# Performance work log

Hardware: AMD Instinct MI355X
Metric: run time of the kernel (lower is better)

Reference implementation:

```python
import jax, jax.numpy as jnp
import numpy as np

N_NODES = 50000
N_EDGES = 800000
IN_CH = 128
HID = 64
HEADS = 4
OUT_CH = 10
NUM_GRAPHS = 500
NEG_SLOPE = 0.2  # PyG GATConv default LeakyReLU slope


def gat_conv(x, src, dst, W, a_src, a_dst, b, concat):
    """One PyG-style GATConv (inference; attention dropout disabled).
    x: [N, F_in], src/dst: [E'] (self-loops already appended).
    W: [F_in, H*C], a_src/a_dst: [H, C], b: [H*C] or [C].
    """
    N = x.shape[0]
    H, C = a_src.shape
    h = (x @ W).reshape(N, H, C)                      # [N,H,C]
    al_s = jnp.einsum('nhc,hc->nh', h, a_src)          # [N,H]
    al_d = jnp.einsum('nhc,hc->nh', h, a_dst)          # [N,H]
    e = al_s[src] + al_d[dst]                          # [E,H]
    e = jnp.where(e > 0, e, NEG_SLOPE * e)             # leaky_relu
    # segment softmax over edges sharing the same destination node
    e_max = jax.ops.segment_max(e, dst, num_segments=N)
    ex = jnp.exp(e - e_max[dst])
    denom = jax.ops.segment_sum(ex, dst, num_segments=N)
    alpha = ex / (denom[dst] + 1e-16)                  # [E,H]
    msg = h[src] * alpha[:, :, None]                   # [E,H,C]
    out = jax.ops.segment_sum(msg, dst, num_segments=N)  # [N,H,C]
    out = out.reshape(N, H * C) if concat else out.mean(axis=1)
    return out + b


def _forward(x, edge_index, batch, W1, a_src1, a_dst1, b1,
             W2, a_src2, a_dst2, b2, fc_w, fc_b):
    N = x.shape[0]
    loops = jnp.arange(N, dtype=edge_index.dtype)
    src = jnp.concatenate([edge_index[0], loops])
    dst = jnp.concatenate([edge_index[1], loops])
    h = gat_conv(x, src, dst, W1, a_src1, a_dst1, b1, concat=True)
    h = jax.nn.relu(h)                                  # dropout: eval mode
    h = gat_conv(h, src, dst, W2, a_src2, a_dst2, b2, concat=False)
    pooled = jax.ops.segment_sum(h, batch, num_segments=NUM_GRAPHS)  # global_add_pool
    logits = pooled @ fc_w + fc_b
    return jax.nn.log_softmax(logits, axis=1)


def setup_inputs() -> dict:
    key = jax.random.key(0)
    ks = jax.random.split(key, 12)
    g = lambda k, shp, fan: jax.random.normal(k, shp, dtype=jnp.float32) * (1.0 / np.sqrt(fan))
    x = jax.random.normal(ks[0], (N_NODES, IN_CH), dtype=jnp.float32)
    edge_index = jax.random.randint(ks[1], (2, N_EDGES), 0, N_NODES, dtype=jnp.int64)
    batch = jnp.sort(jax.random.randint(ks[2], (N_NODES,), 0, NUM_GRAPHS, dtype=jnp.int64))
    return {
        'x': x,
        'edge_index': edge_index,
        'batch': batch,
        'W1': g(ks[3], (IN_CH, HEADS * HID), IN_CH),
        'a_src1': g(ks[4], (HEADS, HID), HID),
        'a_dst1': g(ks[5], (HEADS, HID), HID),
        'b1': jnp.zeros((HEADS * HID,), dtype=jnp.float32),
        'W2': g(ks[6], (HEADS * HID, HID), HEADS * HID),
        'a_src2': g(ks[7], (1, HID), HID),
        'a_dst2': g(ks[8], (1, HID), HID),
        'b2': jnp.zeros((HID,), dtype=jnp.float32),
        'fc_w': g(ks[9], (HID, OUT_CH), HID),
        'fc_b': jnp.zeros((OUT_CH,), dtype=jnp.float32),
    }


def reference(x, edge_index, batch, W1, a_src1, a_dst1, b1,
              W2, a_src2, a_dst2, b2, fc_w, fc_b):
    return _forward(x, edge_index, batch, W1, a_src1, a_dst1, b1,
                    W2, a_src2, a_dst2, b2, fc_w, fc_b)
```

## Files before the change

kernel.cpp:

```cpp
#include <hip/hip_runtime.h>
#include <hip/hip_fp16.h>
#include <math.h>

#define N_NODES   50000
#define N_EDGES   800000
#define IN_CH     128
#define HID       64
#define HEADS     4
#define F1        (HEADS * HID)
#define OUT_CH    10
#define NUM_GRAPHS 500
#define NEG_SLOPE 0.2f
#define RPAD      132
#define NTILES    (N_NODES / 16)
#define CAP       64

typedef __attribute__((ext_vector_type(8))) _Float16 half8;
typedef __attribute__((ext_vector_type(4))) float floatx4;

__device__ __forceinline__ unsigned short f2h(float f) {
    _Float16 h = (_Float16)f;
    unsigned short u; __builtin_memcpy(&u, &h, 2); return u;
}
__device__ __forceinline__ unsigned int pack_h2(float lo, float hi) {
    auto r = __builtin_amdgcn_cvt_pkrtz(lo, hi);
    unsigned int u; __builtin_memcpy(&u, &r, 4); return u;
}
__device__ __forceinline__ float h2f(unsigned short u) {
    _Float16 h; __builtin_memcpy(&h, &u, 2); return (float)h;
}

__global__ void init_kernel(int* __restrict__ cnt, unsigned short* __restrict__ csr,
                            const float* __restrict__ W1, unsigned short* __restrict__ W1p,
                            const float* __restrict__ W2, unsigned short* __restrict__ W2p)
{
    const int gid = blockIdx.x * blockDim.x + threadIdx.x;
    if (gid < N_NODES) {
        cnt[gid] = 1;
        csr[gid * CAP] = (unsigned short)gid;
    }
    if (gid < 4096) {
        const int t = gid >> 8, kt = (gid >> 6) & 3, l = gid & 63;
        const int col = t * 16 + (l & 15);
        unsigned short* o = W1p + (size_t)((t * 4 + kt) * 64 + l) * 8;
        #pragma unroll
        for (int j = 0; j < 8; ++j) {
            const int k = kt * 32 + (l >> 4) * 8 + j;
            o[j] = f2h(W1[k * F1 + col]);
        }
    } else if (gid < 6144) {
        const int g2 = gid - 4096;
        const int t = g2 >> 9, kt = (g2 >> 6) & 7, l = g2 & 63;
        const int col = t * 16 + (l & 15);
        unsigned short* o = W2p + (size_t)((t * 8 + kt) * 64 + l) * 8;
        #pragma unroll
        for (int j = 0; j < 8; ++j) {
            const int k = kt * 32 + (l >> 4) * 8 + j;
            o[j] = f2h(W2[k * HID + col]);
        }
    }
}

__global__ __launch_bounds__(256) void scatter_gemm1(
    const int* __restrict__ ei, int* __restrict__ cnt,
    unsigned short* __restrict__ csr,
    const float* __restrict__ x, const unsigned short* __restrict__ W1p,
    const float* __restrict__ a_src1, const float* __restrict__ a_dst1,
    unsigned short* __restrict__ H1b,
    float* __restrict__ al_s1, float* __restrict__ al_d1)
{
    const int e = blockIdx.x * 256 + threadIdx.x;
    const int src = ei[e];
    const int dst = ei[N_EDGES + e];
    const int slot = atomicAdd(&cnt[dst], 1);

    const int m0 = blockIdx.x * 16;
    const int w = threadIdx.x >> 6;
    const int l = threadIdx.x & 63;
    const int q = l >> 4, r = l & 15;
    floatx4 acc[4] = {};
    const float* arow = x + (size_t)(m0 + r) * IN_CH + q * 8;
    #pragma unroll
    for (int kt = 0; kt < 4; ++kt) {
        const float4 f0 = *(const float4*)(arow + kt * 32);
        const float4 f1 = *(const float4*)(arow + kt * 32 + 4);
        union { uint4 u; half8 h; } a;
        a.u = make_uint4(pack_h2(f0.x, f0.y), pack_h2(f0.z, f0.w),
                         pack_h2(f1.x, f1.y), pack_h2(f1.z, f1.w));
        #pragma unroll
        for (int t = 0; t < 4; ++t) {
            const int nt = w * 4 + t;
            const half8 b = *(const half8*)(W1p + (size_t)((nt * 4 + kt) * 64 + l) * 8);
            acc[t] = __builtin_amdgcn_mfma_f32_16x16x32_f16(a.h, b, acc[t], 0, 0, 0);
        }
    }
    float ls[4] = {0.f, 0.f, 0.f, 0.f}, ld[4] = {0.f, 0.f, 0.f, 0.f};
    #pragma unroll
    for (int t = 0; t < 4; ++t) {
        const int col = (w * 4 + t) * 16 + r;
        const float as = a_src1[col], ad = a_dst1[col];
        #pragma unroll
        for (int reg = 0; reg < 4; ++reg) {
            H1b[(size_t)(m0 + q * 4 + reg) * F1 + col] = f2h(acc[t][reg]);
            ls[reg] += acc[t][reg] * as;
            ld[reg] += acc[t][reg] * ad;
        }
    }
    #pragma unroll
    for (int reg = 0; reg < 4; ++reg) {
        #pragma unroll
        for (int off = 8; off > 0; off >>= 1) {
            ls[reg] += __shfl_down(ls[reg], off, 16);
            ld[reg] += __shfl_down(ld[reg], off, 16);
        }
    }
    if (r == 0) {
        #pragma unroll
        for (int reg = 0; reg < 4; ++reg) {
            const int n = m0 + q * 4 + reg;
            al_s1[n * HEADS + w] = ls[reg];
            al_d1[n * HEADS + w] = ld[reg];
        }
    }

    if (slot < CAP) csr[dst * CAP + slot] = (unsigned short)src;
}

__global__ __launch_bounds__(256) void agg1_gemm2(
    const int* __restrict__ cnt, const unsigned short* __restrict__ csr,
    const float* __restrict__ al_s1, const float* __restrict__ al_d1,
    const uint2* __restrict__ H1b2, const float* __restrict__ b1,
    const unsigned short* __restrict__ W2p,
    const float* __restrict__ a_src2, const float* __restrict__ a_dst2,
    unsigned short* __restrict__ H2b,
    float* __restrict__ al_s2, float* __restrict__ al_d2)
{
    const int m0 = blockIdx.x * 16;
    const int w = threadIdx.x >> 6;
    const int l = threadIdx.x & 63;
    const char* H1base = (const char*)H1b2;
    __shared__ unsigned int rows[16][RPAD];
    __shared__ unsigned int sofs[16][CAP];
    __shared__ uint2        wtp[16][CAP];

    int nreg[4];
    #pragma unroll
    for (int d = 0; d < 4; ++d) {
        const int dd = w * 4 + d;
        const int dstn = m0 + dd;
        const int n = min(cnt[dstn], CAP);
        nreg[d] = n;
        const float4 ad = *(const float4*)(al_d1 + dstn * 4);
        float w0 = 0.f, w1 = 0.f, w2 = 0.f, w3 = 0.f;
        unsigned int off = 0;
        if (l < n) {
            const int s = csr[dstn * CAP + l];
            off = (unsigned int)s << 9;
            const float4 as = *(const float4*)(al_s1 + s * 4);
            float t0 = as.x + ad.x; t0 = t0 > 0.f ? t0 : NEG_SLOPE * t0;
            float t1 = as.y + ad.y; t1 = t1 > 0.f ? t1 : NEG_SLOPE * t1;
            float t2 = as.z + ad.z; t2 = t2 > 0.f ? t2 : NEG_SLOPE * t2;
            float t3 = as.w + ad.w; t3 = t3 > 0.f ? t3 : NEG_SLOPE * t3;
            w0 = __expf(t0); w1 = __expf(t1); w2 = __expf(t2); w3 = __expf(t3);
        }
        sofs[dd][l] = off;
        wtp[dd][l] = make_uint2(pack_h2(w0, w1), pack_h2(w2, w3));
    }
    __syncthreads();

    const int hf = l >> 5;
    const int ll = l & 31;
    const int hh = ll >> 3;
    const unsigned int lane16 = (unsigned int)(ll * 16);
    const float4 bb0 = *(const float4*)(b1 + 8 * ll);
    const float4 bb4 = *(const float4*)(b1 + 8 * ll + 4);
    #pragma unroll 1
    for (int d = 0; d < 4; ++d) {
        const int dd = w * 4 + d;
        const int n = nreg[d];
        float a0=0.f,a1=0.f,a2=0.f,a3=0.f,a4=0.f,a5=0.f,a6=0.f,a7=0.f,den=0.f;
        const int n8 = (n + 7) & ~7;
        for (int i = 0; i < n8; i += 8) {
            unsigned int off[4]; float wt[4];
            #pragma unroll
            for (int j = 0; j < 4; ++j) {
                const int slot = i + 2 * j + hf;
                off[j] = sofs[dd][slot];
                const uint2 wp = wtp[dd][slot];
                const unsigned int uw = (hh & 2) ? wp.y : wp.x;
                wt[j] = h2f((hh & 1) ? (unsigned short)(uw >> 16)
                                     : (unsigned short)(uw & 0xFFFFu));
            }
            uint4 u[4];
            #pragma unroll
            for (int j = 0; j < 4; ++j)
                u[j] = *(const uint4*)(H1base + (off[j] + lane16));
            #pragma unroll
            for (int j = 0; j < 4; ++j) {
                union { uint4 v; _Float16 hv[8]; } c; c.v = u[j];
                a0 += wt[j] * (float)c.hv[0];
                a1 += wt[j] * (float)c.hv[1];
                a2 += wt[j] * (float)c.hv[2];
                a3 += wt[j] * (float)c.hv[3];
                a4 += wt[j] * (float)c.hv[4];
                a5 += wt[j] * (float)c.hv[5];
                a6 += wt[j] * (float)c.hv[6];
                a7 += wt[j] * (float)c.hv[7];
                den += wt[j];
            }
        }
        a0 += __shfl_xor(a0, 32, 64);
        a1 += __shfl_xor(a1, 32, 64);
        a2 += __shfl_xor(a2, 32, 64);
        a3 += __shfl_xor(a3, 32, 64);
        a4 += __shfl_xor(a4, 32, 64);
        a5 += __shfl_xor(a5, 32, 64);
        a6 += __shfl_xor(a6, 32, 64);
        a7 += __shfl_xor(a7, 32, 64);
        den += __shfl_xor(den, 32, 64);
        if (l < 32) {
            const float rcp = 1.f / (den + 1e-16f);
            float v0 = fmaxf(a0 * rcp + bb0.x, 0.f);
            float v1 = fmaxf(a1 * rcp + bb0.y, 0.f);
            float v2 = fmaxf(a2 * rcp + bb0.z, 0.f);
            float v3 = fmaxf(a3 * rcp + bb0.w, 0.f);
            float v4 = fmaxf(a4 * rcp + bb4.x, 0.f);
            float v5 = fmaxf(a5 * rcp + bb4.y, 0.f);
            float v6 = fmaxf(a6 * rcp + bb4.z, 0.f);
            float v7 = fmaxf(a7 * rcp + bb4.w, 0.f);
            *(uint4*)&rows[dd][4 * ll] = make_uint4(pack_h2(v0, v1), pack_h2(v2, v3),
                                                    pack_h2(v4, v5), pack_h2(v6, v7));
        }
    }
    __syncthreads();

    const int q = l >> 4, r = l & 15;
    floatx4 acc = {};
    #pragma unroll
    for (int kt = 0; kt < 8; ++kt) {
        union { uint4 u; half8 hh2; } a;
        a.u = *(const uint4*)&rows[r][kt * 16 + q * 4];
        const half8 b = *(const half8*)(W2p + (size_t)((w * 8 + kt) * 64 + l) * 8);
        acc = __builtin_amdgcn_mfma_f32_16x16x32_f16(a.hh2, b, acc, 0, 0, 0);
    }
    const int col = w * 16 + r;
    const float as = a_src2[col], ad2 = a_dst2[col];
    float ls[4], ld[4];
    #pragma unroll
    for (int reg = 0; reg < 4; ++reg) {
        H2b[(size_t)(m0 + q * 4 + reg) * HID + col] = f2h(acc[reg]);
        ls[reg] = acc[reg] * as;
        ld[reg] = acc[reg] * ad2;
    }
    #pragma unroll
    for (int reg = 0; reg < 4; ++reg) {
        #pragma unroll
        for (int off = 8; off > 0; off >>= 1) {
            ls[reg] += __shfl_down(ls[reg], off, 16);
            ld[reg] += __shfl_down(ld[reg], off, 16);
        }
    }
    __shared__ float Ls[4][16], Ld[4][16];
    if (r == 0) {
        #pragma unroll
        for (int reg = 0; reg < 4; ++reg) {
            Ls[w][q * 4 + reg] = ls[reg];
            Ld[w][q * 4 + reg] = ld[reg];
        }
    }
    __syncthreads();
    if (threadIdx.x < 16) {
        const int row = threadIdx.x;
        al_s2[m0 + row] = Ls[0][row] + Ls[1][row] + Ls[2][row] + Ls[3][row];
        al_d2[m0 + row] = Ld[0][row] + Ld[1][row] + Ld[2][row] + Ld[3][row];
    }
}

__global__ __launch_bounds__(256) void agg2_csr(
    const int* __restrict__ cnt, const unsigned short* __restrict__ csr,
    const float* __restrict__ al_s2, const float* __restrict__ al_d2,
    const uint2* __restrict__ H2b2, uint2* __restrict__ out2b)
{
    const int dst = blockIdx.x * 4 + (threadIdx.x >> 6);
    const int l = threadIdx.x & 63;
    const int qt = l >> 4, j = l & 15;
    const int n = min(cnt[dst], CAP);
    const float ad = al_d2[dst];
    float a0 = 0.f, a1 = 0.f, a2 = 0.f, a3 = 0.f, den = 0.f;
    int s_reg = 0;
    float w_reg = 0.f;
    if (l < n) {
        s_reg = csr[dst * CAP + l];
        float t = al_s2[s_reg] + ad;
        t = t > 0.f ? t : NEG_SLOPE * t;
        w_reg = __expf(t);
    }
    const int n8 = (n + 7) & ~7;
    for (int i = 0; i < n8; i += 8) {
        const int e0 = i + qt, e1 = i + 4 + qt;
        const int   src0 = __shfl(s_reg, e0, 64), src1 = __shfl(s_reg, e1, 64);
        const float wt0  = __shfl(w_reg, e0, 64), wt1  = __shfl(w_reg, e1, 64);
        const uint2 u0 = H2b2[(size_t)src0 * (HID / 4) + j];
        const uint2 u1 = H2b2[(size_t)src1 * (HID / 4) + j];
        union { uint2 v; _Float16 hv[4]; } c0, c1; c0.v = u0; c1.v = u1;
        a0 += wt0 * (float)c0.hv[0] + wt1 * (float)c1.hv[0];
        a1 += wt0 * (float)c0.hv[1] + wt1 * (float)c1.hv[1];
        a2 += wt0 * (float)c0.hv[2] + wt1 * (float)c1.hv[2];
        a3 += wt0 * (float)c0.hv[3] + wt1 * (float)c1.hv[3];
        den += wt0 + wt1;
    }
    #pragma unroll
    for (int m = 16; m <= 32; m <<= 1) {
        a0 += __shfl_xor(a0, m, 64);
        a1 += __shfl_xor(a1, m, 64);
        a2 += __shfl_xor(a2, m, 64);
        a3 += __shfl_xor(a3, m, 64);
        den += __shfl_xor(den, m, 64);
    }
    if (l < 16) {
        const float rcp = 1.f / (den + 1e-16f);
        out2b[(size_t)dst * (HID / 4) + j] =
            make_uint2(pack_h2(a0 * rcp, a1 * rcp), pack_h2(a2 * rcp, a3 * rcp));
    }
}

__global__ __launch_bounds__(256) void pool_fc_kernel(
    const unsigned short* __restrict__ out2b, const float* __restrict__ b2,
    const int* __restrict__ batch,
    const float* __restrict__ fc_w, const float* __restrict__ fc_b,
    float* __restrict__ out)
{
    const int g = blockIdx.x;
    const int q = threadIdx.x >> 6, c = threadIdx.x & 63;
    __shared__ int se[2];
    __shared__ float partial[4][HID];
    __shared__ float pl[HID];
    __shared__ float logits[OUT_CH];
    if (threadIdx.x < 2) {
        const int target = g + threadIdx.x;
        int lo = 0, hi = N_NODES;
        while (lo < hi) { int mid = (lo + hi) >> 1; if (batch[mid] < target) lo = mid + 1; else hi = mid; }
        se[threadIdx.x] = lo;
    }
    __syncthreads();
    const int start = se[0], end = se[1];
    float acc = 0.f;
    for (int n = start + q; n < end; n += 4)
        acc += h2f(out2b[(size_t)n * HID + c]);
    partial[q][c] = acc;
    __syncthreads();
    if (q == 0)
        pl[c] = partial[0][c] + partial[1][c] + partial[2][c] + partial[3][c]
              + (float)(end - start) * b2[c];
    __syncthreads();
    if (threadIdx.x < OUT_CH) {
        float lg = fc_b[threadIdx.x];
        #pragma unroll
        for (int k = 0; k < HID; ++k) lg += pl[k] * fc_w[k * OUT_CH + threadIdx.x];
        logits[threadIdx.x] = lg;
    }
    __syncthreads();
    if (threadIdx.x == 0) {
        float m = logits[0];
        #pragma unroll
        for (int j2 = 1; j2 < OUT_CH; ++j2) m = fmaxf(m, logits[j2]);
        float s = 0.f;
        #pragma unroll
        for (int j2 = 0; j2 < OUT_CH; ++j2) s += __expf(logits[j2] - m);
        const float lse = m + __logf(s);
        #pragma unroll
        for (int j2 = 0; j2 < OUT_CH; ++j2) out[g * OUT_CH + j2] = logits[j2] - lse;
    }
}


extern "C" void kernel_launch(void* const* d_in, const int* in_sizes, int n_in,
                              void* d_out, int out_size, void* d_ws, size_t ws_size,
                              hipStream_t stream)
{
    const float* x      = (const float*)d_in[0];
    const int*   ei     = (const int*)  d_in[1];
    const int*   batch  = (const int*)  d_in[2];
    const float* W1     = (const float*)d_in[3];
    const float* a_src1 = (const float*)d_in[4];
    const float* a_dst1 = (const float*)d_in[5];
    const float* b1     = (const float*)d_in[6];
    const float* W2     = (const float*)d_in[7];
    const float* a_src2 = (const float*)d_in[8];
    const float* a_dst2 = (const float*)d_in[9];
    const float* b2     = (const float*)d_in[10];
    const float* fc_w   = (const float*)d_in[11];
    const float* fc_b   = (const float*)d_in[12];
    float* out = (float*)d_out;

    char* ws = (char*)d_ws;
    size_t off = 0;
    auto alloc_b = [&](size_t bytes) { void* p = (void*)(ws + off); off += (bytes + 15) & ~15ull; return p; };

    unsigned short* H1b  = (unsigned short*)alloc_b((size_t)N_NODES * F1 * 2);
    float* al_s1  = (float*)alloc_b((size_t)N_NODES * HEADS * 4);
    float* al_d1  = (float*)alloc_b((size_t)N_NODES * HEADS * 4);
    unsigned short* H2b  = (unsigned short*)alloc_b((size_t)N_NODES * HID * 2);
    float* al_s2  = (float*)alloc_b((size_t)N_NODES * 4);
    float* al_d2  = (float*)alloc_b((size_t)N_NODES * 4);
    unsigned short* out2b = (unsigned short*)alloc_b((size_t)N_NODES * HID * 2);
    int*   cnt    = (int*)alloc_b((size_t)N_NODES * 4);
    unsigned short* csr = (unsigned short*)alloc_b((size_t)N_NODES * CAP * 2);
    unsigned short* W1p = (unsigned short*)alloc_b((size_t)IN_CH * F1 * 2);
    unsigned short* W2p = (unsigned short*)alloc_b((size_t)F1 * HID * 2);

    init_kernel<<<(N_NODES + 255) / 256, 256, 0, stream>>>(cnt, csr, W1, W1p, W2, W2p);

    scatter_gemm1<<<NTILES, 256, 0, stream>>>(ei, cnt, csr, x, W1p,
                                              a_src1, a_dst1, H1b, al_s1, al_d1);

    agg1_gemm2<<<N_NODES / 16, 256, 0, stream>>>(cnt, csr, al_s1, al_d1,
                                                 (const uint2*)H1b, b1,
                                                 W2p, a_src2, a_dst2,
                                                 H2b, al_s2, al_d2);

    agg2_csr<<<N_NODES / 4, 256, 0, stream>>>(cnt, csr, al_s2, al_d2,
                                              (const uint2*)H2b, (uint2*)out2b);

    pool_fc_kernel<<<NUM_GRAPHS, 256, 0, stream>>>(out2b, b2, batch, fc_w, fc_b, out);
}
```

Baseline: 233.5 us.

## Split per-destination edge buckets into eight segments to spread atomic contention

The single per-node counter and 64-slot adjacency bucket become eight segments, each holding 16 slots, selected by the scatter block index, so atomics on the same destination spread across separate counters. Both aggregation kernels now read eight counters, build a prefix sum, and map each lane to its segment and slot. This aims to cut atomic serialization in the scatter phase. The cost is eight counter loads per destination, a larger initialization, and the risk of dropping edges when one segment exceeds 16 entries.

```diff
diff --git a/kernel.cpp b/kernel.cpp
--- a/kernel.cpp
+++ b/kernel.cpp
@@ -13,7 +13,8 @@
 #define NEG_SLOPE 0.2f
 #define RPAD      132
 #define NTILES    (N_NODES / 16)
-#define CAP       64
+#define NSEG      8
+#define SCAP      16
 
 typedef __attribute__((ext_vector_type(8))) _Float16 half8;
 typedef __attribute__((ext_vector_type(4))) float floatx4;
@@ -30,14 +31,17 @@
     _Float16 h; __builtin_memcpy(&h, &u, 2); return (float)h;
 }
 
-__global__ void init_kernel(int* __restrict__ cnt, unsigned short* __restrict__ csr,
+__global__ void init_kernel(int* __restrict__ cnt2, unsigned short* __restrict__ csr2,
                             const float* __restrict__ W1, unsigned short* __restrict__ W1p,
                             const float* __restrict__ W2, unsigned short* __restrict__ W2p)
 {
     const int gid = blockIdx.x * blockDim.x + threadIdx.x;
     if (gid < N_NODES) {
-        cnt[gid] = 1;
-        csr[gid * CAP] = (unsigned short)gid;
+        const int sseg = gid & 7;
+        #pragma unroll
+        for (int xx = 0; xx < NSEG; ++xx)
+            cnt2[xx * N_NODES + gid] = (xx == sseg) ? 1 : 0;
+        csr2[(sseg * N_NODES + gid) << 4] = (unsigned short)gid;
     }
     if (gid < 4096) {
         const int t = gid >> 8, kt = (gid >> 6) & 3, l = gid & 63;
@@ -62,17 +66,18 @@
 }
 
 __global__ __launch_bounds__(256) void scatter_gemm1(
-    const int* __restrict__ ei, int* __restrict__ cnt,
-    unsigned short* __restrict__ csr,
+    const int* __restrict__ ei, int* __restrict__ cnt2,
+    unsigned short* __restrict__ csr2,
     const float* __restrict__ x, const unsigned short* __restrict__ W1p,
     const float* __restrict__ a_src1, const float* __restrict__ a_dst1,
     unsigned short* __restrict__ H1b,
     float* __restrict__ al_s1, float* __restrict__ al_d1)
 {
     const int e = blockIdx.x * 256 + threadIdx.x;
+    const int seg = blockIdx.x & 7;
     const int src = ei[e];
     const int dst = ei[N_EDGES + e];
-    const int slot = atomicAdd(&cnt[dst], 1);
+    const int slot = atomicAdd(&cnt2[seg * N_NODES + dst], 1);
 
     const int m0 = blockIdx.x * 16;
     const int w = threadIdx.x >> 6;
@@ -123,11 +128,11 @@
         }
     }
 
-    if (slot < CAP) csr[dst * CAP + slot] = (unsigned short)src;
+    if (slot < SCAP) csr2[((seg * N_NODES + dst) << 4) + slot] = (unsigned short)src;
 }
 
 __global__ __launch_bounds__(256) void agg1_gemm2(
-    const int* __restrict__ cnt, const unsigned short* __restrict__ csr,
+    const int* __restrict__ cnt2, const unsigned short* __restrict__ csr2,
     const float* __restrict__ al_s1, const float* __restrict__ al_d1,
     const uint2* __restrict__ H1b2, const float* __restrict__ b1,
     const unsigned short* __restrict__ W2p,
@@ -140,21 +145,29 @@
     const int l = threadIdx.x & 63;
     const char* H1base = (const char*)H1b2;
     __shared__ unsigned int rows[16][RPAD];
-    __shared__ unsigned int sofs[16][CAP];
-    __shared__ uint2        wtp[16][CAP];
+    __shared__ unsigned int sofs[16][64];
+    __shared__ uint2        wtp[16][64];
 
     int nreg[4];
     #pragma unroll
     for (int d = 0; d < 4; ++d) {
         const int dd = w * 4 + d;
         const int dstn = m0 + dd;
-        const int n = min(cnt[dstn], CAP);
+        int pre[NSEG + 1]; pre[0] = 0;
+        #pragma unroll
+        for (int xx = 0; xx < NSEG; ++xx)
+            pre[xx + 1] = pre[xx] + min(cnt2[xx * N_NODES + dstn], SCAP);
+        const int n = min(pre[NSEG], 64);
         nreg[d] = n;
         const float4 ad = *(const float4*)(al_d1 + dstn * 4);
         float w0 = 0.f, w1 = 0.f, w2 = 0.f, w3 = 0.f;
         unsigned int off = 0;
         if (l < n) {
-            const int s = csr[dstn * CAP + l];
+            int x = 0, pb = 0;
+            #pragma unroll
+            for (int yy = 1; yy < NSEG; ++yy)
+                if (l >= pre[yy]) { x = yy; pb = pre[yy]; }
+            const int s = csr2[((x * N_NODES + dstn) << 4) + (l - pb)];
             off = (unsigned int)s << 9;
             const float4 as = *(const float4*)(al_s1 + s * 4);
             float t0 = as.x + ad.x; t0 = t0 > 0.f ? t0 : NEG_SLOPE * t0;
@@ -277,20 +290,28 @@
 }
 
 __global__ __launch_bounds__(256) void agg2_csr(
-    const int* __restrict__ cnt, const unsigned short* __restrict__ csr,
+    const int* __restrict__ cnt2, const unsigned short* __restrict__ csr2,
     const float* __restrict__ al_s2, const float* __restrict__ al_d2,
     const uint2* __restrict__ H2b2, uint2* __restrict__ out2b)
 {
     const int dst = blockIdx.x * 4 + (threadIdx.x >> 6);
     const int l = threadIdx.x & 63;
     const int qt = l >> 4, j = l & 15;
-    const int n = min(cnt[dst], CAP);
+    int pre[NSEG + 1]; pre[0] = 0;
+    #pragma unroll
+    for (int xx = 0; xx < NSEG; ++xx)
+        pre[xx + 1] = pre[xx] + min(cnt2[xx * N_NODES + dst], SCAP);
+    const int n = min(pre[NSEG], 64);
     const float ad = al_d2[dst];
     float a0 = 0.f, a1 = 0.f, a2 = 0.f, a3 = 0.f, den = 0.f;
     int s_reg = 0;
     float w_reg = 0.f;
     if (l < n) {
-        s_reg = csr[dst * CAP + l];
+        int x = 0, pb = 0;
+        #pragma unroll
+        for (int yy = 1; yy < NSEG; ++yy)
+            if (l >= pre[yy]) { x = yy; pb = pre[yy]; }
+        s_reg = csr2[((x * N_NODES + dst) << 4) + (l - pb)];
         float t = al_s2[s_reg] + ad;
         t = t > 0.f ? t : NEG_SLOPE * t;
         w_reg = __expf(t);
@@ -404,22 +425,22 @@
     float* al_s2  = (float*)alloc_b((size_t)N_NODES * 4);
     float* al_d2  = (float*)alloc_b((size_t)N_NODES * 4);
     unsigned short* out2b = (unsigned short*)alloc_b((size_t)N_NODES * HID * 2);
-    int*   cnt    = (int*)alloc_b((size_t)N_NODES * 4);
-    unsigned short* csr = (unsigned short*)alloc_b((size_t)N_NODES * CAP * 2);
+    int*   cnt2   = (int*)alloc_b((size_t)NSEG * N_NODES * 4);
+    unsigned short* csr2 = (unsigned short*)alloc_b((size_t)NSEG * N_NODES * SCAP * 2);
     unsigned short* W1p = (unsigned short*)alloc_b((size_t)IN_CH * F1 * 2);
     unsigned short* W2p = (unsigned short*)alloc_b((size_t)F1 * HID * 2);
 
-    init_kernel<<<(N_NODES + 255) / 256, 256, 0, stream>>>(cnt, csr, W1, W1p, W2, W2p);
-
-    scatter_gemm1<<<NTILES, 256, 0, stream>>>(ei, cnt, csr, x, W1p,
+    init_kernel<<<(N_NODES + 255) / 256, 256, 0, stream>>>(cnt2, csr2, W1, W1p, W2, W2p);
+
+    scatter_gemm1<<<NTILES, 256, 0, stream>>>(ei, cnt2, csr2, x, W1p,
                                               a_src1, a_dst1, H1b, al_s1, al_d1);
 
-    agg1_gemm2<<<N_NODES / 16, 256, 0, stream>>>(cnt, csr, al_s1, al_d1,
+    agg1_gemm2<<<N_NODES / 16, 256, 0, stream>>>(cnt2, csr2, al_s1, al_d1,
                                                  (const uint2*)H1b, b1,
                                                  W2p, a_src2, a_dst2,
                                                  H2b, al_s2, al_d2);
 
-    agg2_csr<<<N_NODES / 4, 256, 0, stream>>>(cnt, csr, al_s2, al_d2,
+    agg2_csr<<<N_NODES / 4, 256, 0, stream>>>(cnt2, csr2, al_s2, al_d2,
                                               (const uint2*)H2b, (uint2*)out2b);
 
     pool_fc_kernel<<<NUM_GRAPHS, 256, 0, stream>>>(out2b, b2, batch, fc_w, fc_b, out);
```

Result: no change. 236.4 us (+1.2%).
